# Performance work log

Hardware: AMD Instinct MI355X
Metric: run time of the kernel (lower is better)

Reference implementation:

```python
import jax, jax.numpy as jnp
import numpy as np

K = 3          # opt.k: number of nearest SOM nodes each point is assigned to
SOM_M = 256    # opt.node_num (16x16 SOM grid)


def _point_resnet(x, ws, bs):
    # SO-Net PointResNet: stack of 1x1 conv (relu) layers; the LAST layer takes
    # concat(prev_out, input) as a residual skip connection.
    out = x
    n = len(ws)
    for i in range(n):
        inp = jnp.concatenate([out, x], axis=1) if i == n - 1 else out
        out = jax.nn.relu(jnp.einsum('oc,bcn->bon', ws[i], inp) + bs[i][None, :, None])
    return out


def _encoder(x, sn, node, fp_ws, fp_bs, fn_ws, fn_bs):
    B, _, N = x.shape
    M = node.shape[2]
    xd = jax.lax.stop_gradient(x)      # torch used x.data throughout SOM logic
    nd = jax.lax.stop_gradient(node)
    # squared distances point->node: B,N,M
    x2 = jnp.sum(xd * xd, axis=1)
    n2 = jnp.sum(nd * nd, axis=1)
    cross = jnp.einsum('bcn,bcm->bnm', xd, nd)
    d2 = x2[:, :, None] + n2[:, None, :] - 2.0 * cross
    _, knn_idx = jax.lax.top_k(-d2, K)                 # B,N,K nearest SOM nodes
    min_idx = jnp.transpose(knn_idx, (0, 2, 1)).reshape(B, K * N)  # B,kN (k-major, matches x_stack)
    x_stack = jnp.tile(x, (1, 1, K))                   # B,3,kN
    xs_d = jax.lax.stop_gradient(x_stack)
    # mask_row_sum (counts per node) and masked sum == one-hot mask multiply in the original
    counts = jax.vmap(lambda s: jax.ops.segment_sum(jnp.ones(s.shape, jnp.float32), s, num_segments=SOM_M))(min_idx)  # B,M
    sums = jax.vmap(lambda d, s: jax.ops.segment_sum(d, s, num_segments=SOM_M))(jnp.transpose(xs_d, (0, 2, 1)), min_idx)  # B,M,3
    cluster_mean = jnp.transpose(sums, (0, 2, 1)) / (counts[:, None, :] + 1e-5)  # B,3,M (new som_node)
    # centers: per-point gather of its assigned node (sum(mask*node) over M)
    centers = jnp.take_along_axis(cluster_mean, min_idx[:, None, :], axis=2)     # B,3,kN
    x_dec = jax.lax.stop_gradient(x_stack - centers)   # .detach() in original
    first = _point_resnet(x_dec, fp_ws, fp_bs)         # B,384,kN
    # index_max + gather: per (b,c,node) max over assigned points; empty nodes -> point index 0
    node_max = jax.vmap(lambda d, s: jax.ops.segment_max(d, s, num_segments=SOM_M))(jnp.transpose(first, (0, 2, 1)), min_idx)  # B,M,C
    node_max = jnp.transpose(node_max, (0, 2, 1))      # B,C,M
    has_pts = counts > 0                               # mask_row_max
    fallback = first[:, :, 0:1]                        # gather index 0 for empty nodes
    masked_max = jnp.where(has_pts[:, None, :], node_max, fallback)  # B,384,M
    final_in = jnp.concatenate([cluster_mean, masked_max], axis=1)   # B,387,M
    final = _point_resnet(final_in, fn_ws, fn_bs)      # B,1024,M
    return jnp.max(final, axis=2)                      # B,1024 global feature


def setup_inputs() -> dict:
    key = jax.random.key(0)
    ks = jax.random.split(key, 24)
    B, N, M = 8, 4096, SOM_M
    inp = {
        'x': jax.random.normal(ks[0], (B, 3, N), jnp.float32),
        'sn': jax.random.normal(ks[1], (B, 3, N), jnp.float32),
        'node': jax.random.normal(ks[2], (B, 3, M), jnp.float32),
        'node_knn_I': jax.random.randint(ks[3], (B, M, 1), 0, M),
    }
    fp_dims = [(3, 64), (64, 128), (128, 256), (256 + 3, 384)]
    fn_dims = [(387, 512), (512, 512), (512, 768), (768 + 387, 1024)]
    i = 4
    for j, (cin, cout) in enumerate(fp_dims):
        inp[f'fp_w{j}'] = jax.random.normal(ks[i], (cout, cin), jnp.float32) * np.float32(np.sqrt(2.0 / cin)); i += 1
        inp[f'fp_b{j}'] = jnp.zeros((cout,), jnp.float32)
    for j, (cin, cout) in enumerate(fn_dims):
        inp[f'fn_w{j}'] = jax.random.normal(ks[i], (cout, cin), jnp.float32) * np.float32(np.sqrt(2.0 / cin)); i += 1
        inp[f'fn_b{j}'] = jnp.zeros((cout,), jnp.float32)
    return inp


def reference(x, sn, node, node_knn_I,
              fp_w0, fp_b0, fp_w1, fp_b1, fp_w2, fp_b2, fp_w3, fp_b3,
              fn_w0, fn_b0, fn_w1, fn_b1, fn_w2, fn_b2, fn_w3, fn_b3):
    fp_ws = [fp_w0, fp_w1, fp_w2, fp_w3]
    fp_bs = [fp_b0, fp_b1, fp_b2, fp_b3]
    fn_ws = [fn_w0, fn_w1, fn_w2, fn_w3]
    fn_bs = [fn_b0, fn_b1, fn_b2, fn_b3]
    # node_knn_I only used when som_k >= 2 (KNNModule); som_k=1 here.
    return _encoder(x, sn, node, fp_ws, fp_bs, fn_ws, fn_bs)
```

## Files before the change

### kernel.cpp

```cpp
#include <hip/hip_runtime.h>
#include <math.h>

#define B_   8
#define N_   4096
#define M_   256
#define KNN_ 3

#define OFF_COUNTS   0
#define OFF_SUMS     2048
#define OFF_CM       8192
#define OFF_NODEMAX  14336
#define OFF_H0       14336
#define OFF_FIRST0   800768
#define OFF_CURSOR   803840
#define ZERO_COUNT   805888
#define OFF_OFFS     805888
#define OFF_KNN      807944
#define OFF_CAT      807944
#define OFF_SORTED   906248
#define OFF_MSORT    1004552
#define OFF_FIN2     2020360
#define OFF_H1       2020360
#define OFF_WBF      2544648
#define OFF_W3X      3661832
#define O_W0 0
#define O_W1 2048
#define O_W2 10240
#define O_W3 43008
#define O_V0 153600
#define O_V1 366592
#define O_V2 628736
#define O_V3 1021952
#define W_TOTAL 2234368

typedef short  bf16x8 __attribute__((ext_vector_type(8)));
typedef float  f32x4  __attribute__((ext_vector_type(4)));

__device__ __forceinline__ unsigned short f2b(float f) {
    unsigned u = __float_as_uint(f);
    return (unsigned short)((u + 0x7FFFu + ((u >> 16) & 1u)) >> 16);
}
__device__ __forceinline__ unsigned cvt2(float lo, float hi) {
    unsigned r;
    asm("v_cvt_pk_bf16_f32 %0, %1, %2" : "=v"(r) : "v"(lo), "v"(hi));
    return r;
}

__global__ __launch_bounds__(256) void knn_setup(
        const float* __restrict__ x, const float* __restrict__ node,
        int* __restrict__ knn, float* __restrict__ counts, float* __restrict__ sums,
        const float* s0, const float* s1, const float* s2, const float* s3,
        const float* s4, const float* s5, const float* s6, const float* s7,
        unsigned short* __restrict__ dst, float* __restrict__ w3x) {
    __shared__ float nd0[M_], nd1[M_], nd2[M_], nn2[M_];
    int t = threadIdx.x;
    if (blockIdx.x < 128) {
        int b = blockIdx.x >> 4, xblk = blockIdx.x & 15;
        {
            float c0 = node[(b * 3 + 0) * M_ + t];
            float c1 = node[(b * 3 + 1) * M_ + t];
            float c2 = node[(b * 3 + 2) * M_ + t];
            nd0[t] = c0; nd1[t] = c1; nd2[t] = c2;
            nn2[t] = c0 * c0 + c1 * c1 + c2 * c2;
        }
        __syncthreads();
        int n = xblk * 256 + t;
        float x0 = x[(b * 3 + 0) * N_ + n];
        float x1 = x[(b * 3 + 1) * N_ + n];
        float x2 = x[(b * 3 + 2) * N_ + n];
        float xx = x0 * x0 + x1 * x1 + x2 * x2;
        float d0 = 1e30f, d1 = 1e30f, d2b = 1e30f;
        int i0 = 0, i1 = 0, i2 = 0;
        for (int m = 0; m < M_; m++) {
            float cross = x0 * nd0[m] + x1 * nd1[m] + x2 * nd2[m];
            float d = xx + nn2[m] - 2.f * cross;
            bool c0 = d < d0, c1 = d < d1, c2 = d < d2b;
            d2b = c1 ? d1 : (c2 ? d : d2b);
            i2  = c1 ? i1 : (c2 ? m : i2);
            d1  = c0 ? d0 : (c1 ? d : d1);
            i1  = c0 ? i0 : (c1 ? m : i1);
            d0  = c0 ? d  : d0;
            i0  = c0 ? m  : i0;
        }
        int base = (b * N_ + n) * 3;
        knn[base + 0] = i0; knn[base + 1] = i1; knn[base + 2] = i2;
        int mm[3] = {i0, i1, i2};
        #pragma unroll
        for (int k = 0; k < 3; k++) {
            int m = mm[k];
            atomicAdd(&counts[b * M_ + m], 1.f);
            atomicAdd(&sums[(b * M_ + m) * 3 + 0], x0);
            atomicAdd(&sums[(b * M_ + m) * 3 + 1], x1);
            atomicAdd(&sums[(b * M_ + m) * 3 + 2], x2);
        }
    } else {
        int i = (blockIdx.x - 128) * 256 + t;
        int st = (gridDim.x - 128) * 256;
        for (int j = i; j < 1536; j += st) {
            int ch = j >> 2, c = j & 3;
            w3x[j] = (c < 3) ? s3[ch * 259 + 256 + c] : 0.f;
        }
        for (; i < W_TOTAL; i += st) {
            const float* src; int base, cin, cinp;
            if      (i < O_W1) { src = s0; base = O_W0; cin = 3;    cinp = 32; }
            else if (i < O_W2) { src = s1; base = O_W1; cin = 64;   cinp = 64; }
            else if (i < O_W3) { src = s2; base = O_W2; cin = 128;  cinp = 128; }
            else if (i < O_V0) { src = s3; base = O_W3; cin = 259;  cinp = 288; }
            else if (i < O_V1) { src = s4; base = O_V0; cin = 387;  cinp = 416; }
            else if (i < O_V2) { src = s5; base = O_V1; cin = 512;  cinp = 512; }
            else if (i < O_V3) { src = s6; base = O_V2; cin = 512;  cinp = 512; }
            else               { src = s7; base = O_V3; cin = 1155; cinp = 1184; }
            int loc = i - base;
            int co = loc / cinp, k = loc - co * cinp;
            dst[i] = (k < cin) ? f2b(src[co * cin + k]) : (unsigned short)0;
        }
    }
}

__global__ __launch_bounds__(256) void cmean_scan(const float* __restrict__ counts,
        const float* __restrict__ sums, float* __restrict__ cm, int* __restrict__ offs) {
    __shared__ int tmp[256];
    int t = threadIdx.x, b = blockIdx.x;
    float cnt = counts[b * M_ + t];
    float inv = 1.f / (cnt + 1e-5f);
    #pragma unroll
    for (int c = 0; c < 3; c++)
        cm[(b * 3 + c) * M_ + t] = sums[(b * M_ + t) * 3 + c] * inv;
    int v = (int)cnt;
    tmp[t] = v;
    __syncthreads();
    for (int off = 1; off < 256; off <<= 1) {
        int u = (t >= off) ? tmp[t - off] : 0;
        __syncthreads();
        tmp[t] += u;
        __syncthreads();
    }
    offs[b * 257 + t] = tmp[t] - v;
    if (t == 255) offs[b * 257 + 256] = tmp[255];
}

__global__ __launch_bounds__(256) void scatter(const int* __restrict__ knn,
        const int* __restrict__ offs, int* __restrict__ cursor,
        int* __restrict__ sorted, int* __restrict__ msort) {
    int g = blockIdx.x * 256 + threadIdx.x;
    int b = g / (KNN_ * N_), j = g % (KNN_ * N_);
    int n = j & (N_ - 1), k = j >> 12;
    int m = knn[(b * N_ + n) * 3 + k];
    int pos = atomicAdd(&cursor[b * M_ + m], 1);
    int dst = offs[b * 257 + m] + pos;
    sorted[b * (KNN_ * N_) + dst] = j;
    msort[b * (KNN_ * N_) + dst] = m;
}

template<int KS, int INS, int OUTS, int CTW>
__device__ __forceinline__ void layerB(const unsigned short* __restrict__ Wg,
        const float* __restrict__ bias, const unsigned short* actin,
        unsigned short* actout, int wave, int lane) {
    int r = lane & 15, g = lane >> 4;
    bf16x8 bfr[4][KS];
    #pragma unroll
    for (int pt = 0; pt < 4; pt++) {
        const unsigned short* arow = actin + (pt * 16 + r) * INS + g * 8;
        #pragma unroll
        for (int ks = 0; ks < KS; ks++)
            bfr[pt][ks] = *(const bf16x8*)(arow + ks * 32);
    }
    #pragma unroll
    for (int c = 0; c < CTW; c++) {
        int ct = wave * CTW + c;
        const unsigned short* wrow = Wg + (ct * 16 + r) * (KS * 32) + g * 8;
        f32x4 acc[4];
        #pragma unroll
        for (int pt = 0; pt < 4; pt++) acc[pt] = (f32x4){0.f, 0.f, 0.f, 0.f};
        #pragma unroll
        for (int ks = 0; ks < KS; ks++) {
            bf16x8 wv = *(const bf16x8*)(wrow + ks * 32);
            #pragma unroll
            for (int pt = 0; pt < 4; pt++)
                acc[pt] = __builtin_amdgcn_mfma_f32_16x16x32_bf16(wv, bfr[pt][ks], acc[pt], 0, 0, 0);
        }
        f32x4 b4 = *(const f32x4*)(bias + ct * 16 + g * 4);
        #pragma unroll
        for (int pt = 0; pt < 4; pt++) {
            uint2 s;
            s.x = cvt2(fmaxf(acc[pt][0] + b4[0], 0.f), fmaxf(acc[pt][1] + b4[1], 0.f));
            s.y = cvt2(fmaxf(acc[pt][2] + b4[2], 0.f), fmaxf(acc[pt][3] + b4[3], 0.f));
            *(uint2*)(actout + (pt * 16 + r) * OUTS + ct * 16 + g * 4) = s;
        }
    }
}

__global__ __launch_bounds__(256, 3) void mlp1m(
        const float* __restrict__ x, const float* __restrict__ cm,
        const int* __restrict__ sorted, const int* __restrict__ msort,
        const unsigned short* __restrict__ wb, const float4* __restrict__ w3x,
        const float* __restrict__ bb0, const float* __restrict__ bb1,
        const float* __restrict__ bb2, const float* __restrict__ bb3,
        float* __restrict__ node_max, float* __restrict__ first0) {
    __shared__ __align__(16) char smem[50688];
    unsigned short* inb = (unsigned short*)smem;
    unsigned short* a1  = (unsigned short*)smem;
    unsigned short* a0  = (unsigned short*)(smem + 16896);
    unsigned short* cat = (unsigned short*)(smem + 16896);
    __shared__ float4 xdf[64];
    __shared__ int midx[64], segm[65], segstart[66];
    __shared__ int nseg, p0loc;
    int t = threadIdx.x, b = blockIdx.y, lane = t & 63, wave = t >> 6;
    int e0 = blockIdx.x * 64;
    for (int e = t; e < 1280; e += 256) ((unsigned*)inb)[e] = 0u;
    __syncthreads();
    if (t < 64) {
        int p = t;
        if (p == 0) p0loc = -1;
        int j = sorted[b * 12288 + e0 + p];
        int m = msort[b * 12288 + e0 + p];
        int n = j & (N_ - 1);
        midx[p] = m;
        float xd0 = x[(b * 3 + 0) * N_ + n] - cm[(b * 3 + 0) * M_ + m];
        float xd1 = x[(b * 3 + 1) * N_ + n] - cm[(b * 3 + 1) * M_ + m];
        float xd2 = x[(b * 3 + 2) * N_ + n] - cm[(b * 3 + 2) * M_ + m];
        xdf[p] = make_float4(xd0, xd1, xd2, 0.f);
        inb[p * 40 + 0] = f2b(xd0);
        inb[p * 40 + 1] = f2b(xd1);
        inb[p * 40 + 2] = f2b(xd2);
        int prev = __shfl_up(m, 1);
        bool flag = (p == 0) || (m != prev);
        unsigned long long mk = __ballot(flag);
        int sid = __popcll(mk & ((1ull << p) - 1ull));
        if (flag) { segstart[sid] = p; segm[sid] = m; }
        if (p == 63) { int ns2 = __popcll(mk); nseg = ns2; segstart[ns2] = 64; }
        if (j == 0) p0loc = p;
    }
    __syncthreads();
    layerB<1, 40, 72, 1>(wb + O_W0, bb0, inb, a0, wave, lane);
    __syncthreads();
    layerB<2, 72, 132, 2>(wb + O_W1, bb1, a0, a1, wave, lane);
    __syncthreads();
    layerB<4, 132, 264, 4>(wb + O_W2, bb2, a1, cat, wave, lane);
    __syncthreads();
    int r = lane & 15, g = lane >> 4;
    bf16x8 bfr[4][8];
    #pragma unroll
    for (int pt = 0; pt < 4; pt++) {
        const unsigned short* arow = cat + (pt * 16 + r) * 264 + g * 8;
        #pragma unroll
        for (int ks = 0; ks < 8; ks++)
            bfr[pt][ks] = *(const bf16x8*)(arow + ks * 32);
    }
    int ns = nseg, p0l = p0loc;
    #pragma unroll
    for (int c = 0; c < 6; c++) {
        int ct = wave * 6 + c;
        const unsigned short* wrow = wb + O_W3 + (ct * 16 + r) * 288 + g * 8;
        f32x4 acc[4];
        #pragma unroll
        for (int pt = 0; pt < 4; pt++) acc[pt] = (f32x4){0.f, 0.f, 0.f, 0.f};
        #pragma unroll
        for (int ks = 0; ks < 8; ks++) {
            bf16x8 wv = *(const bf16x8*)(wrow + ks * 32);
            #pragma unroll
            for (int pt = 0; pt < 4; pt++)
                acc[pt] = __builtin_amdgcn_mfma_f32_16x16x32_bf16(wv, bfr[pt][ks], acc[pt], 0, 0, 0);
        }
        f32x4 b4 = *(const f32x4*)(bb3 + ct * 16 + g * 4);
        float v[4][4];
        #pragma unroll
        for (int i = 0; i < 4; i++) {
            float4 wx = w3x[ct * 16 + g * 4 + i];
            #pragma unroll
            for (int pt = 0; pt < 4; pt++) {
                float4 xv = xdf[pt * 16 + r];
                float s = acc[pt][i] + b4[i] + wx.x * xv.x + wx.y * xv.y + wx.z * xv.z;
                v[pt][i] = fmaxf(s, 0.f);
            }
        }
        if (p0l >= 0) {
            #pragma unroll
            for (int pt = 0; pt < 4; pt++)
                if (p0l == pt * 16 + r) {
                    #pragma unroll
                    for (int i = 0; i < 4; i++)
                        first0[b * 384 + ct * 16 + g * 4 + i] = v[pt][i];
                }
        }
        for (int s = 0; s < ns; s++) {
            int s0 = segstart[s], s1 = segstart[s + 1];
            float mx0 = 0.f, mx1 = 0.f, mx2 = 0.f, mx3 = 0.f;
            #pragma unroll
            for (int pt = 0; pt < 4; pt++) {
                int p = pt * 16 + r;
                bool in = (p >= s0) && (p < s1);
                mx0 = fmaxf(mx0, in ? v[pt][0] : 0.f);
                mx1 = fmaxf(mx1, in ? v[pt][1] : 0.f);
                mx2 = fmaxf(mx2, in ? v[pt][2] : 0.f);
                mx3 = fmaxf(mx3, in ? v[pt][3] : 0.f);
            }
            #pragma unroll
            for (int sh = 1; sh < 16; sh <<= 1) {
                mx0 = fmaxf(mx0, __shfl_xor(mx0, sh));
                mx1 = fmaxf(mx1, __shfl_xor(mx1, sh));
                mx2 = fmaxf(mx2, __shfl_xor(mx2, sh));
                mx3 = fmaxf(mx3, __shfl_xor(mx3, sh));
            }
            if (r == 0) {
                float* dst = &node_max[(size_t)(b * M_ + segm[s]) * 384 + ct * 16 + g * 4];
                atomicMax((int*)(dst + 0), __float_as_int(mx0));
                atomicMax((int*)(dst + 1), __float_as_int(mx1));
                atomicMax((int*)(dst + 2), __float_as_int(mx2));
                atomicMax((int*)(dst + 3), __float_as_int(mx3));
            }
        }
    }
}

__global__ void build_fin2(const float* __restrict__ cm, const float* __restrict__ counts,
                           const float* __restrict__ nmax, const float* __restrict__ first0,
                           unsigned short* __restrict__ fin2, unsigned short* __restrict__ cat) {
    int tot = 2048 * 416;
    int i = blockIdx.x * blockDim.x + threadIdx.x;
    int st = gridDim.x * blockDim.x;
    for (; i < tot; i += st) {
        int n = i / 416, ch = i - n * 416;
        int b = n >> 8, m = n & 255;
        float v = 0.f;
        if (ch < 3) v = cm[(b * 3 + ch) * M_ + m];
        else if (ch < 387)
            v = (counts[n] > 0.f) ? nmax[(size_t)n * 384 + (ch - 3)]
                                  : first0[b * 384 + (ch - 3)];
        unsigned short u = f2b(v);
        fin2[n * 416 + ch] = u;
        cat[(size_t)n * 1184 + 768 + ch] = u;
    }
}

template<int KS, int CTQ>
__global__ __launch_bounds__(256, 2) void nlayer4(const unsigned short* __restrict__ W,
        const float* __restrict__ bias, const unsigned short* __restrict__ actin,
        unsigned short* __restrict__ actout, int outs) {
    int wave = threadIdx.x >> 6, lane = threadIdx.x & 63;
    int id = blockIdx.x * 4 + wave;
    int nt = id / CTQ, cq = id - nt * CTQ;
    int r = lane & 15, g = lane >> 4;
    const unsigned short* arow = actin + (size_t)(nt * 16 + r) * (KS * 32) + g * 8;
    bf16x8 afr[KS];
    #pragma unroll
    for (int ks = 0; ks < KS; ks++) afr[ks] = *(const bf16x8*)(arow + ks * 32);
    const unsigned short* w0 = W + (cq * 64 + r) * (KS * 32) + g * 8;
    f32x4 acc[4];
    #pragma unroll
    for (int c = 0; c < 4; c++) acc[c] = (f32x4){0.f, 0.f, 0.f, 0.f};
    #pragma unroll
    for (int ks = 0; ks < KS; ks++) {
        #pragma unroll
        for (int c = 0; c < 4; c++) {
            bf16x8 wv = *(const bf16x8*)(w0 + c * 16 * KS * 32 + ks * 32);
            acc[c] = __builtin_amdgcn_mfma_f32_16x16x32_bf16(wv, afr[ks], acc[c], 0, 0, 0);
        }
    }
    #pragma unroll
    for (int c = 0; c < 4; c++) {
        f32x4 b4 = *(const f32x4*)(bias + cq * 64 + c * 16 + g * 4);
        uint2 s;
        s.x = cvt2(fmaxf(acc[c][0] + b4[0], 0.f), fmaxf(acc[c][1] + b4[1], 0.f));
        s.y = cvt2(fmaxf(acc[c][2] + b4[2], 0.f), fmaxf(acc[c][3] + b4[3], 0.f));
        *(uint2*)(actout + (size_t)(nt * 16 + r) * outs + cq * 64 + c * 16 + g * 4) = s;
    }
}

template<int KS, int CTQ>
__global__ __launch_bounds__(256, 2) void nlayer_max4(const unsigned short* __restrict__ W,
        const float* __restrict__ bias, const unsigned short* __restrict__ actin,
        float* __restrict__ out) {
    int wave = threadIdx.x >> 6, lane = threadIdx.x & 63;
    int id = blockIdx.x * 4 + wave;
    int nt = id / CTQ, cq = id - nt * CTQ;
    int r = lane & 15, g = lane >> 4;
    const unsigned short* arow = actin + (size_t)(nt * 16 + r) * (KS * 32) + g * 8;
    bf16x8 afr[KS];
    #pragma unroll
    for (int ks = 0; ks < KS; ks++) afr[ks] = *(const bf16x8*)(arow + ks * 32);
    const unsigned short* w0 = W + (cq * 64 + r) * (KS * 32) + g * 8;
    f32x4 acc[4];
    #pragma unroll
    for (int c = 0; c < 4; c++) acc[c] = (f32x4){0.f, 0.f, 0.f, 0.f};
    #pragma unroll
    for (int ks = 0; ks < KS; ks++) {
        #pragma unroll
        for (int c = 0; c < 4; c++) {
            bf16x8 wv = *(const bf16x8*)(w0 + c * 16 * KS * 32 + ks * 32);
            acc[c] = __builtin_amdgcn_mfma_f32_16x16x32_bf16(wv, afr[ks], acc[c], 0, 0, 0);
        }
    }
    int b = nt >> 4;
    #pragma unroll
    for (int c = 0; c < 4; c++) {
        f32x4 b4 = *(const f32x4*)(bias + cq * 64 + c * 16 + g * 4);
        #pragma unroll
        for (int i = 0; i < 4; i++) {
            float v = fmaxf(acc[c][i] + b4[i], 0.f);
            v = fmaxf(v, __shfl_xor(v, 1));
            v = fmaxf(v, __shfl_xor(v, 2));
            v = fmaxf(v, __shfl_xor(v, 4));
            v = fmaxf(v, __shfl_xor(v, 8));
            if (r == 0)
                atomicMax((int*)&out[b * 1024 + cq * 64 + c * 16 + g * 4 + i],
                          __float_as_int(v));
        }
    }
}

extern "C" void kernel_launch(void* const* d_in, const int* in_sizes, int n_in,
                              void* d_out, int out_size, void* d_ws, size_t ws_size,
                              hipStream_t stream) {
    (void)in_sizes; (void)n_in; (void)out_size; (void)ws_size;
    const float* x    = (const float*)d_in[0];
    const float* node = (const float*)d_in[2];
    const float* fpw[4] = {(const float*)d_in[4], (const float*)d_in[6],
                           (const float*)d_in[8], (const float*)d_in[10]};
    const float* fpb[4] = {(const float*)d_in[5], (const float*)d_in[7],
                           (const float*)d_in[9], (const float*)d_in[11]};
    const float* fnw[4] = {(const float*)d_in[12], (const float*)d_in[14],
                           (const float*)d_in[16], (const float*)d_in[18]};
    const float* fnb[4] = {(const float*)d_in[13], (const float*)d_in[15],
                           (const float*)d_in[17], (const float*)d_in[19]};
    float* ws  = (float*)d_ws;
    float* out = (float*)d_out;
    unsigned short* wb   = (unsigned short*)(ws + OFF_WBF);
    unsigned short* fin2 = (unsigned short*)(ws + OFF_FIN2);
    unsigned short* h0   = (unsigned short*)(ws + OFF_H0);
    unsigned short* h1   = (unsigned short*)(ws + OFF_H1);
    unsigned short* catb = (unsigned short*)(ws + OFF_CAT);

    hipMemsetAsync(ws, 0, (size_t)ZERO_COUNT * 4, stream);
    hipMemsetAsync(out, 0, (size_t)B_ * 1024 * 4, stream);

    knn_setup<<<128 + 2048, 256, 0, stream>>>(
        x, node, (int*)(ws + OFF_KNN), ws + OFF_COUNTS, ws + OFF_SUMS,
        fpw[0], fpw[1], fpw[2], fpw[3], fnw[0], fnw[1], fnw[2], fnw[3],
        wb, ws + OFF_W3X);
    cmean_scan<<<B_, 256, 0, stream>>>(
        ws + OFF_COUNTS, ws + OFF_SUMS, ws + OFF_CM, (int*)(ws + OFF_OFFS));
    scatter<<<B_ * KNN_ * N_ / 256, 256, 0, stream>>>(
        (int*)(ws + OFF_KNN), (int*)(ws + OFF_OFFS), (int*)(ws + OFF_CURSOR),
        (int*)(ws + OFF_SORTED), (int*)(ws + OFF_MSORT));
    mlp1m<<<dim3(KNN_ * N_ / 64, B_), 256, 0, stream>>>(
        x, ws + OFF_CM, (int*)(ws + OFF_SORTED), (int*)(ws + OFF_MSORT), wb,
        (const float4*)(ws + OFF_W3X),
        fpb[0], fpb[1], fpb[2], fpb[3], ws + OFF_NODEMAX, ws + OFF_FIRST0);
    build_fin2<<<3328, 256, 0, stream>>>(
        ws + OFF_CM, ws + OFF_COUNTS, ws + OFF_NODEMAX, ws + OFF_FIRST0, fin2, catb);
    nlayer4<13, 8><<<256,  256, 0, stream>>>(wb + O_V0, fnb[0], fin2, h0, 512);
    nlayer4<16, 8><<<256,  256, 0, stream>>>(wb + O_V1, fnb[1], h0, h1, 512);
    nlayer4<16, 12><<<384, 256, 0, stream>>>(wb + O_V2, fnb[2], h1, catb, 1184);
    nlayer_max4<37, 16><<<512, 256, 0, stream>>>(wb + O_V3, fnb[3], catb, out);
}
```

Before: 232.4 us.

## Use 32x32x16 MFMA with points on rows for last first-MLP layer

Rewrites the final layer of the first point MLP to use 32x32x16 bf16 MFMA with points as the M dimension and output channels as N. Each wave computes all 64 points times 96 channels at once. The transposed accumulator layout puts channels across lanes, so the per-segment max needs only one cross-half shuffle instead of a 16-lane butterfly. Atomics become lane-contiguous per channel. It trades higher accumulator register pressure (96 floats) for fewer shuffles and more MFMA work per instruction, and may hurt occupancy at launch bound 3.

```diff
diff --git a/kernel.cpp b/kernel.cpp
--- a/kernel.cpp
+++ b/kernel.cpp
@@ -35,6 +35,7 @@
 
 typedef short  bf16x8 __attribute__((ext_vector_type(8)));
 typedef float  f32x4  __attribute__((ext_vector_type(4)));
+typedef float  f32x16 __attribute__((ext_vector_type(16)));
 
 __device__ __forceinline__ unsigned short f2b(float f) {
     unsigned u = __float_as_uint(f);
@@ -44,6 +45,12 @@
     unsigned r;
     asm("v_cvt_pk_bf16_f32 %0, %1, %2" : "=v"(r) : "v"(lo), "v"(hi));
     return r;
+}
+__device__ __forceinline__ f32x16 zero16() {
+    f32x16 z;
+    #pragma unroll
+    for (int i = 0; i < 16; i++) z[i] = 0.f;
+    return z;
 }
 
 __global__ __launch_bounds__(256) void knn_setup(
@@ -203,7 +210,7 @@
     unsigned short* a0  = (unsigned short*)(smem + 16896);
     unsigned short* cat = (unsigned short*)(smem + 16896);
     __shared__ float4 xdf[64];
-    __shared__ int midx[64], segm[65], segstart[66];
+    __shared__ int segm[65], segstart[66];
     __shared__ int nseg, p0loc;
     int t = threadIdx.x, b = blockIdx.y, lane = t & 63, wave = t >> 6;
     int e0 = blockIdx.x * 64;
@@ -215,7 +222,6 @@
         int j = sorted[b * 12288 + e0 + p];
         int m = msort[b * 12288 + e0 + p];
         int n = j & (N_ - 1);
-        midx[p] = m;
         float xd0 = x[(b * 3 + 0) * N_ + n] - cm[(b * 3 + 0) * M_ + m];
         float xd1 = x[(b * 3 + 1) * N_ + n] - cm[(b * 3 + 1) * M_ + m];
         float xd2 = x[(b * 3 + 2) * N_ + n] - cm[(b * 3 + 2) * M_ + m];
@@ -238,77 +244,91 @@
     __syncthreads();
     layerB<4, 132, 264, 4>(wb + O_W2, bb2, a1, cat, wave, lane);
     __syncthreads();
-    int r = lane & 15, g = lane >> 4;
-    bf16x8 bfr[4][8];
-    #pragma unroll
-    for (int pt = 0; pt < 4; pt++) {
-        const unsigned short* arow = cat + (pt * 16 + r) * 264 + g * 8;
-        #pragma unroll
-        for (int ks = 0; ks < 8; ks++)
-            bfr[pt][ks] = *(const bf16x8*)(arow + ks * 32);
+    int l31 = lane & 31, half = lane >> 5;
+    f32x16 acc[6];
+    #pragma unroll
+    for (int q = 0; q < 6; q++) acc[q] = zero16();
+    {
+        const unsigned short* arow0 = cat + l31 * 264 + half * 8;
+        const unsigned short* arow1 = cat + (32 + l31) * 264 + half * 8;
+        const unsigned short* wrowb = wb + O_W3 + (wave * 96 + l31) * 288 + half * 8;
+        #pragma unroll
+        for (int ks = 0; ks < 16; ks++) {
+            bf16x8 aA = *(const bf16x8*)(arow0 + ks * 16);
+            bf16x8 aB = *(const bf16x8*)(arow1 + ks * 16);
+            #pragma unroll
+            for (int c3 = 0; c3 < 3; c3++) {
+                bf16x8 wv = *(const bf16x8*)(wrowb + c3 * 32 * 288 + ks * 16);
+                acc[c3 * 2 + 0] = __builtin_amdgcn_mfma_f32_32x32x16_bf16(aA, wv, acc[c3 * 2 + 0], 0, 0, 0);
+                acc[c3 * 2 + 1] = __builtin_amdgcn_mfma_f32_32x32x16_bf16(aB, wv, acc[c3 * 2 + 1], 0, 0, 0);
+            }
+        }
     }
     int ns = nseg, p0l = p0loc;
-    #pragma unroll
-    for (int c = 0; c < 6; c++) {
-        int ct = wave * 6 + c;
-        const unsigned short* wrow = wb + O_W3 + (ct * 16 + r) * 288 + g * 8;
-        f32x4 acc[4];
-        #pragma unroll
-        for (int pt = 0; pt < 4; pt++) acc[pt] = (f32x4){0.f, 0.f, 0.f, 0.f};
-        #pragma unroll
-        for (int ks = 0; ks < 8; ks++) {
-            bf16x8 wv = *(const bf16x8*)(wrow + ks * 32);
-            #pragma unroll
-            for (int pt = 0; pt < 4; pt++)
-                acc[pt] = __builtin_amdgcn_mfma_f32_16x16x32_bf16(wv, bfr[pt][ks], acc[pt], 0, 0, 0);
-        }
-        f32x4 b4 = *(const f32x4*)(bb3 + ct * 16 + g * 4);
-        float v[4][4];
-        #pragma unroll
-        for (int i = 0; i < 4; i++) {
-            float4 wx = w3x[ct * 16 + g * 4 + i];
-            #pragma unroll
-            for (int pt = 0; pt < 4; pt++) {
-                float4 xv = xdf[pt * 16 + r];
-                float s = acc[pt][i] + b4[i] + wx.x * xv.x + wx.y * xv.y + wx.z * xv.z;
-                v[pt][i] = fmaxf(s, 0.f);
+    float bias3[3]; float4 wx3[3];
+    #pragma unroll
+    for (int c3 = 0; c3 < 3; c3++) {
+        bias3[c3] = bb3[(wave * 3 + c3) * 32 + l31];
+        wx3[c3]   = w3x[(wave * 3 + c3) * 32 + l31];
+    }
+    #pragma unroll
+    for (int ph = 0; ph < 2; ph++) {
+        #pragma unroll
+        for (int rg = 0; rg < 16; rg++) {
+            int row = ph * 32 + (rg & 3) + 8 * (rg >> 2) + 4 * half;
+            float4 xv = xdf[row];
+            #pragma unroll
+            for (int c3 = 0; c3 < 3; c3++) {
+                float s = acc[c3 * 2 + ph][rg] + bias3[c3]
+                        + wx3[c3].x * xv.x + wx3[c3].y * xv.y + wx3[c3].z * xv.z;
+                acc[c3 * 2 + ph][rg] = fmaxf(s, 0.f);
             }
         }
-        if (p0l >= 0) {
-            #pragma unroll
-            for (int pt = 0; pt < 4; pt++)
-                if (p0l == pt * 16 + r) {
+    }
+    if (p0l >= 0) {
+        #pragma unroll
+        for (int ph = 0; ph < 2; ph++)
+            #pragma unroll
+            for (int rg = 0; rg < 16; rg++) {
+                int row = ph * 32 + (rg & 3) + 8 * (rg >> 2) + 4 * half;
+                if (row == p0l) {
                     #pragma unroll
-                    for (int i = 0; i < 4; i++)
-                        first0[b * 384 + ct * 16 + g * 4 + i] = v[pt][i];
+                    for (int c3 = 0; c3 < 3; c3++)
+                        first0[b * 384 + (wave * 3 + c3) * 32 + l31] = acc[c3 * 2 + ph][rg];
                 }
-        }
-        for (int s = 0; s < ns; s++) {
-            int s0 = segstart[s], s1 = segstart[s + 1];
-            float mx0 = 0.f, mx1 = 0.f, mx2 = 0.f, mx3 = 0.f;
-            #pragma unroll
-            for (int pt = 0; pt < 4; pt++) {
-                int p = pt * 16 + r;
-                bool in = (p >= s0) && (p < s1);
-                mx0 = fmaxf(mx0, in ? v[pt][0] : 0.f);
-                mx1 = fmaxf(mx1, in ? v[pt][1] : 0.f);
-                mx2 = fmaxf(mx2, in ? v[pt][2] : 0.f);
-                mx3 = fmaxf(mx3, in ? v[pt][3] : 0.f);
             }
-            #pragma unroll
-            for (int sh = 1; sh < 16; sh <<= 1) {
-                mx0 = fmaxf(mx0, __shfl_xor(mx0, sh));
-                mx1 = fmaxf(mx1, __shfl_xor(mx1, sh));
-                mx2 = fmaxf(mx2, __shfl_xor(mx2, sh));
-                mx3 = fmaxf(mx3, __shfl_xor(mx3, sh));
+    }
+    for (int s = 0; s < ns; s++) {
+        int s0 = segstart[s], s1 = segstart[s + 1];
+        float m0 = 0.f, m1 = 0.f, m2 = 0.f;
+        if (s0 < 32) {
+            #pragma unroll
+            for (int rg = 0; rg < 16; rg++) {
+                int row = (rg & 3) + 8 * (rg >> 2) + 4 * half;
+                bool in = (row >= s0) && (row < s1);
+                m0 = fmaxf(m0, in ? acc[0][rg] : 0.f);
+                m1 = fmaxf(m1, in ? acc[2][rg] : 0.f);
+                m2 = fmaxf(m2, in ? acc[4][rg] : 0.f);
             }
-            if (r == 0) {
-                float* dst = &node_max[(size_t)(b * M_ + segm[s]) * 384 + ct * 16 + g * 4];
-                atomicMax((int*)(dst + 0), __float_as_int(mx0));
-                atomicMax((int*)(dst + 1), __float_as_int(mx1));
-                atomicMax((int*)(dst + 2), __float_as_int(mx2));
-                atomicMax((int*)(dst + 3), __float_as_int(mx3));
+        }
+        if (s1 > 32) {
+            #pragma unroll
+            for (int rg = 0; rg < 16; rg++) {
+                int row = 32 + (rg & 3) + 8 * (rg >> 2) + 4 * half;
+                bool in = (row >= s0) && (row < s1);
+                m0 = fmaxf(m0, in ? acc[1][rg] : 0.f);
+                m1 = fmaxf(m1, in ? acc[3][rg] : 0.f);
+                m2 = fmaxf(m2, in ? acc[5][rg] : 0.f);
             }
+        }
+        m0 = fmaxf(m0, __shfl_xor(m0, 32));
+        m1 = fmaxf(m1, __shfl_xor(m1, 32));
+        m2 = fmaxf(m2, __shfl_xor(m2, 32));
+        if (lane < 32) {
+            float* dstp = &node_max[(size_t)(b * M_ + segm[s]) * 384 + wave * 96];
+            atomicMax((int*)(dstp + l31),      __float_as_int(m0));
+            atomicMax((int*)(dstp + 32 + l31), __float_as_int(m1));
+            atomicMax((int*)(dstp + 64 + l31), __float_as_int(m2));
         }
     }
 }
```

Result: faster. 194.5 us (-16.3%).
